# Performance work log

Measured on AMD Instinct MI355X. Metric: run time of the kernel, lower is better.

## Reference

```python
import jax, jax.numpy as jnp
import numpy as np

WS = 8        # window size (square)
TW = 8        # total windows per side = input_resolution // WS
NH = 16       # num heads


def make_indices(ws, tw):
    # local relative position index (N, N)
    c = np.stack(np.meshgrid(np.arange(ws), np.arange(ws), indexing='ij')).reshape(2, -1)
    rel = (c[:, :, None] - c[:, None, :]).transpose(1, 2, 0).astype(np.int64)
    rel[..., 0] += ws - 1
    rel[..., 1] += ws - 1
    rel[..., 0] *= 2 * ws - 1
    local_idx = rel.sum(-1)
    # global (window-token -> window-grid) relative position index (N, tw*tw)
    ck = np.stack(np.meshgrid(np.arange(tw), np.arange(tw), indexing='ij')).reshape(2, -1)
    relg = (c[:, :, None] - ck[:, None, :]).transpose(1, 2, 0).astype(np.int64)
    relg[..., 0] += tw - 1
    relg[..., 1] += tw - 1
    relg[..., 0] *= ws + tw - 1
    global_idx = relg.sum(-1)
    return local_idx, global_idx


def setup_inputs() -> dict:
    key = jax.random.key(0)
    ks = jax.random.split(key, 13)
    B, H, W, C = 16, 64, 64, 512
    s = 0.02
    return {
        'x': jax.random.normal(ks[0], (B, H, W, C), jnp.float32),
        'qkv_w': jax.random.normal(ks[1], (C, 3 * C), jnp.float32) * s,
        'qkv_b': jax.random.normal(ks[2], (3 * C,), jnp.float32) * s,
        'local_bias_table': jax.random.normal(ks[3], ((2 * WS - 1) ** 2, NH), jnp.float32) * s,
        'global_bias_table': jax.random.normal(ks[4], ((WS + TW - 1) ** 2, NH), jnp.float32) * s,
        'local_proj_w': jax.random.normal(ks[5], (C, C), jnp.float32) * s,
        'local_proj_b': jax.random.normal(ks[6], (C,), jnp.float32) * s,
        'pool_w': jnp.full((WS * WS,), 1.0 / (WS * WS) * (WS * WS), jnp.float32) * 0 + jax.random.normal(ks[7], (WS * WS,), jnp.float32) * s + 1.0 / (WS * WS),
        'pool_b': jnp.zeros((1,), jnp.float32),
        'global_proj_w': jax.random.normal(ks[8], (C, C), jnp.float32) * s,
        'global_proj_b': jax.random.normal(ks[9], (C,), jnp.float32) * s,
        'pfc_w': jax.random.normal(ks[10], (2 * C, C), jnp.float32) * s,
        'pfc_b': jax.random.normal(ks[11], (C,), jnp.float32) * s,
    }


def reference(x, qkv_w, qkv_b, local_bias_table, global_bias_table,
              local_proj_w, local_proj_b, pool_w, pool_b,
              global_proj_w, global_proj_b, pfc_w, pfc_b):
    B, H, W, C = x.shape
    N = WS * WS                      # tokens per window
    nWs = (H // WS) * (W // WS)      # number of windows
    B_ = B * nWs
    hd = C // NH
    scale = hd ** -0.5

    local_idx, global_idx = make_indices(WS, H // WS)

    # NOTE: faithful to original — qkv applied to x in row-major order,
    # then reshaped into (B_, N, ...) chunks (window_partition output is unused).
    qkv = (x.reshape(-1, C) @ qkv_w + qkv_b).reshape(B_, N, 3, NH, hd)
    qkv = qkv.transpose(2, 0, 3, 1, 4)  # (3, B_, NH, N, hd)
    q, k, v = qkv[0], qkv[1], qkv[2]

    # ---- fine (local window) attention ----
    lb = local_bias_table[local_idx.reshape(-1)].reshape(N, N, NH).transpose(2, 0, 1)
    fine = jax.nn.softmax(jnp.einsum('bhnd,bhmd->bhnm', q * scale, k) + lb[None])
    fine_out = jnp.einsum('bhnm,bhmd->bnhd', fine, v).reshape(B_, N, C)
    fine_out = fine_out @ local_proj_w + local_proj_b

    # ---- coarse (pooled global) attention ----
    k5 = k.reshape(B, nWs, NH, N, hd)
    v5 = v.reshape(B, nWs, NH, N, hd)
    # pooled over the N window-token axis; original uses pool_layer_k for BOTH K and V
    Kg = jnp.einsum('bwhnd,n->bhwd', k5, pool_w) + pool_b  # (B, NH, nWs, hd)
    Vg = jnp.einsum('bwhnd,n->bhwd', v5, pool_w) + pool_b
    Kb = jnp.broadcast_to(Kg[:, None], (B, nWs, NH, nWs, hd)).reshape(B_, NH, nWs, hd)
    Vb = jnp.broadcast_to(Vg[:, None], (B, nWs, NH, nWs, hd)).reshape(B_, NH, nWs, hd)

    gb = global_bias_table[global_idx.reshape(-1)].reshape(N, nWs, NH).transpose(2, 0, 1)
    coarse = jax.nn.softmax(jnp.einsum('bhnd,bhwd->bhnw', q * scale, Kb) + gb[None])
    coarse_out = jnp.einsum('bhnw,bhwd->bnhd', coarse, Vb).reshape(B_, N, C)
    coarse_out = coarse_out @ global_proj_w + global_proj_b

    # ---- fused projection ----
    out = jnp.concatenate([fine_out, coarse_out], axis=-1) @ pfc_w + pfc_b
    return out  # (B_, N, C)
```

## Files before the change

kernel.cpp:

```cpp
#include <hip/hip_runtime.h>


typedef unsigned int u32;
typedef _Float16 f16;
typedef __attribute__((ext_vector_type(8))) _Float16 f16x8;
typedef __attribute__((ext_vector_type(4))) float f32x4;
typedef __attribute__((ext_vector_type(4))) u32 u32x4;

__device__ __forceinline__ f32x4 mfma_16x16x32(f16x8 a, f16x8 b, f32x4 c) {
  return __builtin_amdgcn_mfma_f32_16x16x32_f16(a, b, c, 0, 0, 0);
}

__device__ __forceinline__ void async_cp16(const void* g, void* l) {
  __builtin_amdgcn_global_load_lds(
      (const __attribute__((address_space(1))) u32*)g,
      (__attribute__((address_space(3))) u32*)l, 16, 0, 0);
}

__device__ __forceinline__ f16x8 cvt8_rtz(const float4 a, const float4 b) {
  u32x4 w;
  w[0] = __builtin_bit_cast(u32, __builtin_amdgcn_cvt_pkrtz(a.x, a.y));
  w[1] = __builtin_bit_cast(u32, __builtin_amdgcn_cvt_pkrtz(a.z, a.w));
  w[2] = __builtin_bit_cast(u32, __builtin_amdgcn_cvt_pkrtz(b.x, b.y));
  w[3] = __builtin_bit_cast(u32, __builtin_amdgcn_cvt_pkrtz(b.z, b.w));
  return __builtin_bit_cast(f16x8, w);
}


__global__ void k_cvtx(const float* __restrict__ X, f16* __restrict__ X16) {
  const size_t stride = (size_t)2048 * 256 * 8;
  size_t base = ((size_t)blockIdx.x * 256 + threadIdx.x) * 8;
  for (int it = 0; it < 8; ++it, base += stride) {
    const float4 a = *reinterpret_cast<const float4*>(X + base);
    const float4 b = *reinterpret_cast<const float4*>(X + base + 4);
    *reinterpret_cast<f16x8*>(X16 + base) = cvt8_rtz(a, b);
  }
}

__global__ void k_biastab(const float* __restrict__ ltab, const float* __restrict__ gtab,
                          float* __restrict__ lbf, float* __restrict__ gbf) {
  const int id = blockIdx.x * 256 + threadIdx.x;
  const int tab = id >> 14;
  const int rem = id & 16383;
  const int h = rem >> 10;
  const int wv = (rem >> 8) & 3;
  const int j = (rem >> 6) & 3;
  const int l = rem & 63;
  const int lk = l >> 4, lr = l & 15;
  const float* src = tab ? gtab : ltab;
  float* out = (tab ? gbf : lbf) + (size_t)rem * 4;
#pragma unroll
  for (int r = 0; r < 4; ++r) {
    const int n = wv * 16 + lk * 4 + r;
    const int m = j * 16 + lr;
    const int idx = ((n >> 3) - (m >> 3) + 7) * 15 + ((n & 7) - (m & 7) + 7);
    out[r] = src[idx * 16 + h];
  }
}

__global__ void k_tqkvw(const float* __restrict__ w, f16* __restrict__ wT) {
  __shared__ f16 sT[64][72];
  const int bid = blockIdx.x;
  const int k0 = (bid / 24) * 64, n0 = (bid % 24) * 64;
  const float sc = (n0 < 512) ? 0.17677669529663687f : 1.0f;
  const int t = threadIdx.x;
#pragma unroll
  for (int p = 0; p < 4; ++p) {
    const int kl = p * 16 + (t >> 4), nl = (t & 15) * 4;
    const float4 v = *reinterpret_cast<const float4*>(w + (size_t)(k0 + kl) * 1536 + n0 + nl);
    sT[kl][nl] = (f16)(v.x * sc); sT[kl][nl + 1] = (f16)(v.y * sc);
    sT[kl][nl + 2] = (f16)(v.z * sc); sT[kl][nl + 3] = (f16)(v.w * sc);
  }
  __syncthreads();
#pragma unroll
  for (int q = 0; q < 2; ++q) {
    const int nl = q * 32 + (t >> 3), kl = (t & 7) * 8;
    f16x8 r;
#pragma unroll
    for (int j = 0; j < 8; ++j) r[j] = sT[kl + j][nl];
    *reinterpret_cast<f16x8*>(wT + (size_t)(n0 + nl) * 512 + k0 + kl) = r;
  }
}

__global__ __launch_bounds__(256) void k_compose(const float* __restrict__ lpw,
                                                 const float* __restrict__ gpw,
                                                 const float* __restrict__ pfc_w,
                                                 f16* __restrict__ WT) {
  __shared__ float sW[16][16];
  const int kk0 = blockIdx.x * 16;
  const bool top = kk0 < 512;
  const float* src = top ? (lpw + kk0 * 512) : (gpw + (kk0 - 512) * 512);
  const float* pf = pfc_w + (top ? 0 : 512 * 512);
  const int t = threadIdx.x;
  float acc0[16], acc1[16];
#pragma unroll
  for (int i = 0; i < 16; ++i) { acc0[i] = 0.f; acc1[i] = 0.f; }
  for (int ct = 0; ct < 32; ++ct) {
    sW[t >> 4][t & 15] = src[(t >> 4) * 512 + ct * 16 + (t & 15)];
    __syncthreads();
#pragma unroll
    for (int cc = 0; cc < 16; ++cc) {
      const int c = ct * 16 + cc;
      const float p0 = pf[c * 512 + t];
      const float p1 = pf[c * 512 + t + 256];
#pragma unroll
      for (int i = 0; i < 16; ++i) { acc0[i] += sW[i][cc] * p0; acc1[i] += sW[i][cc] * p1; }
    }
    __syncthreads();
  }
#pragma unroll
  for (int i = 0; i < 16; ++i) {
    const int kk = kk0 + i;
    const int kp = ((kk >> 5) & 15) * 64 + (kk >> 9) * 32 + (kk & 31);
    WT[(size_t)t * 1024 + kp] = (f16)acc0[i];
    WT[(size_t)(t + 256) * 1024 + kp] = (f16)acc1[i];
  }
}

__global__ void k_bc_init(const float* __restrict__ pfc_b, float* __restrict__ bc) {
  const int j = blockIdx.x * 256 + threadIdx.x;
  bc[j] = pfc_b[j];
}

__global__ void k_bc_acc(const float* __restrict__ lpb, const float* __restrict__ gpb,
                         const float* __restrict__ pfc_w, float* __restrict__ bc) {
  const int t = threadIdx.x;
  const int c0 = blockIdx.x * 32;
  float p0 = 0.f, p1 = 0.f;
#pragma unroll
  for (int i = 0; i < 32; ++i) {
    const int c = c0 + i;
    const float wgt = (c < 512) ? lpb[c] : gpb[c - 512];
    p0 += wgt * pfc_w[(size_t)c * 512 + t];
    p1 += wgt * pfc_w[(size_t)c * 512 + t + 256];
  }
  atomicAdd(bc + t, p0);
  atomicAdd(bc + t + 256, p1);
}

__global__ __launch_bounds__(512, 2) void k_gemm_qkv(const f16* __restrict__ A,
                                                     const f16* __restrict__ BT,
                                                     const float* __restrict__ qkv_b,
                                                     const float* __restrict__ pool_w,
                                                     const float* __restrict__ pool_b,
                                                     f16* __restrict__ qb,
                                                     f16* __restrict__ kb,
                                                     f16* __restrict__ vb,
                                                     f16* __restrict__ Kgb,
                                                     f16* __restrict__ Vgt) {
  __shared__ f16 sA[8192], sB[4096];
  const int wid = (blockIdx.x & 7) * 384 + (blockIdx.x >> 3);
  const int br = wid / 12, bn = wid % 12;
  const int t = threadIdx.x;
  const int wv = t >> 6, l = t & 63, lr = l & 15, lk = l >> 4;
  const int wvr = wv >> 1, wvc = wv & 1;

  f32x4 acc[4][4] = {};

  const f16* gA = A + (size_t)(br * 256 + (t >> 2)) * 512 + (t & 3) * 8;
  const f16* gB = BT + (size_t)(bn * 128 + (t >> 2)) * 512 + (t & 3) * 8;

  for (int kk = 0; kk < 16; ++kk) {
    async_cp16(gA + kk * 32, &sA[t * 8]);
    async_cp16(gA + 128 * 512 + kk * 32, &sA[4096 + t * 8]);
    async_cp16(gB + kk * 32, &sB[t * 8]);
    __syncthreads();
    f16x8 af[4], bf[4];
#pragma unroll
    for (int m = 0; m < 4; ++m)
      af[m] = *reinterpret_cast<const f16x8*>(&sA[(wvr * 64 + m * 16 + lr) * 32 + lk * 8]);
#pragma unroll
    for (int n = 0; n < 4; ++n)
      bf[n] = *reinterpret_cast<const f16x8*>(&sB[(wvc * 64 + n * 16 + lr) * 32 + lk * 8]);
#pragma unroll
    for (int m = 0; m < 4; ++m)
#pragma unroll
      for (int n = 0; n < 4; ++n) acc[m][n] = mfma_16x16x32(af[m], bf[n], acc[m][n]);
    __syncthreads();
  }

  const int w_idx = br * 4 + wvr;
  const int bb = w_idx >> 6, ww = w_idx & 63;
  float pw[4][4];
#pragma unroll
  for (int m = 0; m < 4; ++m)
#pragma unroll
    for (int r = 0; r < 4; ++r) pw[m][r] = pool_w[m * 16 + lk * 4 + r];
  const float pb = pool_b[0];

#pragma unroll
  for (int n = 0; n < 4; ++n) {
    const int col = bn * 128 + wvc * 64 + n * 16 + lr;
    const int which = col >> 9;
    const int hh = (col >> 5) & 15, d = col & 31;
    const float bias = which == 0 ? qkv_b[col] * 0.17677669529663687f : qkv_b[col];
    f16* dst = which == 0 ? qb : (which == 1 ? kb : vb);
#pragma unroll
    for (int m = 0; m < 4; ++m)
#pragma unroll
      for (int r = 0; r < 4; ++r) {
        const int row = br * 256 + wvr * 64 + m * 16 + lk * 4 + r;
        dst[(size_t)(((row >> 6) << 4) + hh) * 2048 + (row & 63) * 32 + d] =
            (f16)(acc[m][n][r] + bias);
      }
    if (which != 0) {
      float part = 0.f;
#pragma unroll
      for (int m = 0; m < 4; ++m)
#pragma unroll
        for (int r = 0; r < 4; ++r) part += (acc[m][n][r] + bias) * pw[m][r];
      part += __shfl_xor(part, 16);
      part += __shfl_xor(part, 32);
      part += pb;
      if (lk == 0) {
        if (which == 1)
          Kgb[((size_t)(bb * 16 + hh) * 64 + ww) * 32 + d] = (f16)part;
        else
          Vgt[((size_t)(bb * 16 + hh) * 32 + d) * 64 + ww] = (f16)part;
      }
    }
  }
}

__global__ __launch_bounds__(256) void k_attn(const f16* __restrict__ qb,
                                              const f16* __restrict__ kb,
                                              const f16* __restrict__ vb,
                                              const f16* __restrict__ Kgb,
                                              const f16* __restrict__ Vgt,
                                              const float* __restrict__ lbf,
                                              const float* __restrict__ gbf,
                                              f16* __restrict__ cat) {
  __shared__ f16 sVraw[2048];
  __shared__ f16 sVt[2048];
  __shared__ f16 sP[4096];
  __shared__ f16 sCat[4096];
  const int bid = blockIdx.x;
  const int b_ = bid >> 4, h = bid & 15;
  const int gs = ((b_ >> 6) << 4) + h;
  const int t = threadIdx.x;
  const int wv = t >> 6, l = t & 63, lr = l & 15, lk = l >> 4;
  const size_t hs = (size_t)bid * 2048;

  async_cp16(vb + hs + t * 8, &sVraw[t * 8]);

  const f16x8 aq = *reinterpret_cast<const f16x8*>(qb + hs + (wv * 16 + lr) * 32 + lk * 8);
  const float* btL = lbf + (size_t)((h * 4 + wv) * 4) * 256 + l * 4;
  const float* btG = gbf + (size_t)((h * 4 + wv) * 4) * 256 + l * 4;

  f32x4 s[4];
#pragma unroll
  for (int j = 0; j < 4; ++j) {
    const f16x8 bk = *reinterpret_cast<const f16x8*>(kb + hs + (j * 16 + lr) * 32 + lk * 8);
    s[j] = mfma_16x16x32(aq, bk, *reinterpret_cast<const f32x4*>(btL + j * 256));
  }

  __syncthreads();

  {
    const int d = t >> 3, tok0 = (t & 7) << 3;
    f16x8 w;
#pragma unroll
    for (int j = 0; j < 8; ++j) w[j] = sVraw[(tok0 + j) * 32 + d];
    *reinterpret_cast<f16x8*>(&sVt[d * 64 + (((t & 7) ^ (d & 7)) << 3)]) = w;
  }

  float p[4][4], inv[4];
#pragma unroll
  for (int r = 0; r < 4; ++r) {
    float su = 0.f;
#pragma unroll
    for (int j = 0; j < 4; ++j) {
      const float e = __expf(s[j][r]);
      p[j][r] = e;
      su += e;
    }
    su += __shfl_xor(su, 1);
    su += __shfl_xor(su, 2);
    su += __shfl_xor(su, 4);
    su += __shfl_xor(su, 8);
    inv[r] = 1.f / su;
  }
#pragma unroll
  for (int r = 0; r < 4; ++r) {
    const int rowP = wv * 16 + lk * 4 + r;
#pragma unroll
    for (int j = 0; j < 4; ++j) {
      const int col = j * 16 + lr;
      sP[rowP * 64 + (((col >> 3) ^ (rowP & 7)) << 3) + (col & 7)] = (f16)p[j][r];
    }
  }

  __syncthreads();

  {
    const int rowP = wv * 16 + lr;
    const f16x8 a0 = *reinterpret_cast<const f16x8*>(&sP[rowP * 64 + ((lk ^ (lr & 7)) << 3)]);
    const f16x8 a1 = *reinterpret_cast<const f16x8*>(&sP[rowP * 64 + (((4 + lk) ^ (lr & 7)) << 3)]);
#pragma unroll
    for (int n = 0; n < 2; ++n) {
      const int d = n * 16 + lr;
      const f16x8 b0 = *reinterpret_cast<const f16x8*>(&sVt[d * 64 + ((lk ^ (d & 7)) << 3)]);
      const f16x8 b1 = *reinterpret_cast<const f16x8*>(&sVt[d * 64 + (((4 + lk) ^ (d & 7)) << 3)]);
      f32x4 o = {};
      o = mfma_16x16x32(a0, b0, o);
      o = mfma_16x16x32(a1, b1, o);
#pragma unroll
      for (int r = 0; r < 4; ++r) {
        const int rowC = wv * 16 + lk * 4 + r;
        const int colC = n * 16 + lr;
        sCat[rowC * 64 + (((colC >> 3) ^ (rowC & 7)) << 3) + (colC & 7)] =
            (f16)(o[r] * inv[r]);
      }
    }
  }

#pragma unroll
  for (int j = 0; j < 4; ++j) {
    const f16x8 bk = *reinterpret_cast<const f16x8*>(
        Kgb + ((size_t)gs * 64 + j * 16 + lr) * 32 + lk * 8);
    s[j] = mfma_16x16x32(aq, bk, *reinterpret_cast<const f32x4*>(btG + j * 256));
  }
#pragma unroll
  for (int r = 0; r < 4; ++r) {
    float su = 0.f;
#pragma unroll
    for (int j = 0; j < 4; ++j) {
      const float e = __expf(s[j][r]);
      p[j][r] = e;
      su += e;
    }
    su += __shfl_xor(su, 1);
    su += __shfl_xor(su, 2);
    su += __shfl_xor(su, 4);
    su += __shfl_xor(su, 8);
    inv[r] = 1.f / su;
  }
#pragma unroll
  for (int r = 0; r < 4; ++r) {
    const int rowP = wv * 16 + lk * 4 + r;
#pragma unroll
    for (int j = 0; j < 4; ++j) {
      const int col = j * 16 + lr;
      sP[rowP * 64 + (((col >> 3) ^ (rowP & 7)) << 3) + (col & 7)] = (f16)p[j][r];
    }
  }

  {
    const int rowP = wv * 16 + lr;
    const f16x8 a0 = *reinterpret_cast<const f16x8*>(&sP[rowP * 64 + ((lk ^ (lr & 7)) << 3)]);
    const f16x8 a1 = *reinterpret_cast<const f16x8*>(&sP[rowP * 64 + (((4 + lk) ^ (lr & 7)) << 3)]);
#pragma unroll
    for (int n = 0; n < 2; ++n) {
      const f16* vp = Vgt + ((size_t)gs * 32 + n * 16 + lr) * 64 + lk * 8;
      const f16x8 b0 = *reinterpret_cast<const f16x8*>(vp);
      const f16x8 b1 = *reinterpret_cast<const f16x8*>(vp + 32);
      f32x4 o = {};
      o = mfma_16x16x32(a0, b0, o);
      o = mfma_16x16x32(a1, b1, o);
#pragma unroll
      for (int r = 0; r < 4; ++r) {
        const int rowC = wv * 16 + lk * 4 + r;
        const int colC = 32 + n * 16 + lr;
        sCat[rowC * 64 + (((colC >> 3) ^ (rowC & 7)) << 3) + (colC & 7)] =
            (f16)(o[r] * inv[r]);
      }
    }
  }

  f16* catp = cat + ((size_t)b_ * 64) * 1024 + h * 64;
#pragma unroll
  for (int pass = 0; pass < 2; ++pass) {
    const int row = wv * 16 + pass * 8 + (l >> 3);
    const int c = l & 7;
    const f16x8 v = *reinterpret_cast<const f16x8*>(&sCat[row * 64 + ((c ^ (row & 7)) << 3)]);
    *reinterpret_cast<f16x8*>(catp + (size_t)row * 1024 + c * 8) = v;
  }
}

__global__ __launch_bounds__(512, 2) void k_gemm_final(const f16* __restrict__ A,
                                                       const f16* __restrict__ BT,
                                                       const float* __restrict__ bc,
                                                       float* __restrict__ out) {
  __shared__ f16 sA[8192];
  __shared__ f16 sB[16384];
  const int wid = (blockIdx.x & 7) * 128 + (blockIdx.x >> 3);
  const int br = wid >> 1, bn = wid & 1;
  const int t = threadIdx.x;
  const int wv = t >> 6, l = t & 63, lr = l & 15, lk = l >> 4;
  const int wvM = wv >> 2, wvN = wv & 3;

  f32x4 acc[4][4] = {};

  const int srow = t >> 3;
  const int scg = (t & 7) ^ (srow & 7);
  const f16* gA = A + (size_t)(br * 128 + srow) * 1024 + scg * 8;
  const f16* gB = BT + (size_t)(bn * 256 + srow) * 1024 + scg * 8;

  for (int kk = 0; kk < 16; ++kk) {
#pragma unroll
    for (int i = 0; i < 2; ++i)
      async_cp16(gA + (size_t)(i * 64) * 1024 + kk * 64, &sA[(i * 512 + t) * 8]);
#pragma unroll
    for (int i = 0; i < 4; ++i)
      async_cp16(gB + (size_t)(i * 64) * 1024 + kk * 64, &sB[(i * 512 + t) * 8]);
    __syncthreads();
    f16x8 af[4][2], bf[4][2];
#pragma unroll
    for (int m = 0; m < 4; ++m) {
      const int row = wvM * 64 + m * 16 + lr;
#pragma unroll
      for (int hh = 0; hh < 2; ++hh)
        af[m][hh] = *reinterpret_cast<const f16x8*>(
            &sA[row * 64 + ((((hh << 2) + lk) ^ (row & 7)) << 3)]);
    }
#pragma unroll
    for (int n = 0; n < 4; ++n) {
      const int row = wvN * 64 + n * 16 + lr;
#pragma unroll
      for (int hh = 0; hh < 2; ++hh)
        bf[n][hh] = *reinterpret_cast<const f16x8*>(
            &sB[row * 64 + ((((hh << 2) + lk) ^ (row & 7)) << 3)]);
    }
#pragma unroll
    for (int m = 0; m < 4; ++m)
#pragma unroll
      for (int n = 0; n < 4; ++n) {
        acc[m][n] = mfma_16x16x32(af[m][0], bf[n][0], acc[m][n]);
        acc[m][n] = mfma_16x16x32(af[m][1], bf[n][1], acc[m][n]);
      }
    __syncthreads();
  }

#pragma unroll
  for (int n = 0; n < 4; ++n) {
    const int col = bn * 256 + wvN * 64 + n * 16 + lr;
    const float bias = bc[col];
#pragma unroll
    for (int m = 0; m < 4; ++m)
#pragma unroll
      for (int r = 0; r < 4; ++r) {
        const int row = br * 128 + wvM * 64 + m * 16 + lk * 4 + r;
        out[(size_t)row * 512 + col] = acc[m][n][r] + bias;
      }
  }
}


extern "C" void kernel_launch(void* const* d_in, const int* in_sizes, int n_in,
                              void* d_out, int out_size, void* d_ws, size_t ws_size,
                              hipStream_t stream) {
  const float* x      = (const float*)d_in[0];
  const float* qkv_w  = (const float*)d_in[1];
  const float* qkv_b  = (const float*)d_in[2];
  const float* ltab   = (const float*)d_in[3];
  const float* gtab   = (const float*)d_in[4];
  const float* lpw    = (const float*)d_in[5];
  const float* lpb    = (const float*)d_in[6];
  const float* pool_w = (const float*)d_in[7];
  const float* pool_b = (const float*)d_in[8];
  const float* gpw    = (const float*)d_in[9];
  const float* gpb    = (const float*)d_in[10];
  const float* pfc_w  = (const float*)d_in[11];
  const float* pfc_b  = (const float*)d_in[12];
  float* out = (float*)d_out;

  char* ws = (char*)d_ws;
  f16*   qb   = (f16*)(ws + 0);
  f16*   kb   = (f16*)(ws + 67108864);
  f16*   vb   = (f16*)(ws + 134217728);
  f16*   cat  = (f16*)(ws + 201326592);
  f16*   X16  = (f16*)(ws + 201326592);
  f16*   qwT  = (f16*)(ws + 335544320);
  f16*   WcT  = (f16*)(ws + 337117184);
  float* bc   = (float*)(ws + 338165760);
  float* lbf  = (float*)(ws + 338167808);
  float* gbf  = (float*)(ws + 338429952);
  f16*   Kgb  = (f16*)(ws + 338692096);
  f16*   Vgt  = (f16*)(ws + 339740672);

  k_cvtx<<<2048, 256, 0, stream>>>(x, X16);
  k_biastab<<<128, 256, 0, stream>>>(ltab, gtab, lbf, gbf);
  k_tqkvw<<<192, 256, 0, stream>>>(qkv_w, qwT);
  k_compose<<<64, 256, 0, stream>>>(lpw, gpw, pfc_w, WcT);
  k_bc_init<<<2, 256, 0, stream>>>(pfc_b, bc);
  k_bc_acc<<<32, 256, 0, stream>>>(lpb, gpb, pfc_w, bc);
  k_gemm_qkv<<<3072, 512, 0, stream>>>(X16, qwT, qkv_b, pool_w, pool_b,
                                       qb, kb, vb, Kgb, Vgt);
  k_attn<<<16384, 256, 0, stream>>>(qb, kb, vb, Kgb, Vgt, lbf, gbf, cat);
  k_gemm_final<<<1024, 512, 0, stream>>>(cat, WcT, bc, out);
}
```

Measured before the change: 484.9 us.

## Merge prep kernels, double-buffer QKV GEMM, process two windows per attention block

New measurement: 449.6 us. -7.3%, faster.

```diff
diff --git a/kernel.cpp b/kernel.cpp
--- a/kernel.cpp
+++ b/kernel.cpp
@@ -26,116 +26,103 @@
   return __builtin_bit_cast(f16x8, w);
 }
 
-
-__global__ void k_cvtx(const float* __restrict__ X, f16* __restrict__ X16) {
-  const size_t stride = (size_t)2048 * 256 * 8;
-  size_t base = ((size_t)blockIdx.x * 256 + threadIdx.x) * 8;
-  for (int it = 0; it < 8; ++it, base += stride) {
-    const float4 a = *reinterpret_cast<const float4*>(X + base);
-    const float4 b = *reinterpret_cast<const float4*>(X + base + 4);
-    *reinterpret_cast<f16x8*>(X16 + base) = cvt8_rtz(a, b);
-  }
-}
-
-__global__ void k_biastab(const float* __restrict__ ltab, const float* __restrict__ gtab,
-                          float* __restrict__ lbf, float* __restrict__ gbf) {
-  const int id = blockIdx.x * 256 + threadIdx.x;
-  const int tab = id >> 14;
-  const int rem = id & 16383;
-  const int h = rem >> 10;
-  const int wv = (rem >> 8) & 3;
-  const int j = (rem >> 6) & 3;
-  const int l = rem & 63;
-  const int lk = l >> 4, lr = l & 15;
-  const float* src = tab ? gtab : ltab;
-  float* out = (tab ? gbf : lbf) + (size_t)rem * 4;
-#pragma unroll
-  for (int r = 0; r < 4; ++r) {
-    const int n = wv * 16 + lk * 4 + r;
-    const int m = j * 16 + lr;
-    const int idx = ((n >> 3) - (m >> 3) + 7) * 15 + ((n & 7) - (m & 7) + 7);
-    out[r] = src[idx * 16 + h];
-  }
-}
-
-__global__ void k_tqkvw(const float* __restrict__ w, f16* __restrict__ wT) {
-  __shared__ f16 sT[64][72];
-  const int bid = blockIdx.x;
-  const int k0 = (bid / 24) * 64, n0 = (bid % 24) * 64;
-  const float sc = (n0 < 512) ? 0.17677669529663687f : 1.0f;
+__global__ __launch_bounds__(256) void k_prep(
+    const float* __restrict__ X, f16* __restrict__ X16,
+    const float* __restrict__ ltab, const float* __restrict__ gtab,
+    float* __restrict__ lbf, float* __restrict__ gbf,
+    const float* __restrict__ qkv_w, f16* __restrict__ qwT,
+    const float* __restrict__ lpw, const float* __restrict__ gpw,
+    const float* __restrict__ pfc_w, f16* __restrict__ WcT,
+    const float* __restrict__ lpb, const float* __restrict__ gpb,
+    const float* __restrict__ pfc_b, float* __restrict__ bc) {
+  __shared__ char sm[9216];
+  const int b = blockIdx.x;
   const int t = threadIdx.x;
-#pragma unroll
-  for (int p = 0; p < 4; ++p) {
-    const int kl = p * 16 + (t >> 4), nl = (t & 15) * 4;
-    const float4 v = *reinterpret_cast<const float4*>(w + (size_t)(k0 + kl) * 1536 + n0 + nl);
-    sT[kl][nl] = (f16)(v.x * sc); sT[kl][nl + 1] = (f16)(v.y * sc);
-    sT[kl][nl + 2] = (f16)(v.z * sc); sT[kl][nl + 3] = (f16)(v.w * sc);
-  }
-  __syncthreads();
-#pragma unroll
-  for (int q = 0; q < 2; ++q) {
-    const int nl = q * 32 + (t >> 3), kl = (t & 7) * 8;
-    f16x8 r;
-#pragma unroll
-    for (int j = 0; j < 8; ++j) r[j] = sT[kl + j][nl];
-    *reinterpret_cast<f16x8*>(wT + (size_t)(n0 + nl) * 512 + k0 + kl) = r;
-  }
-}
-
-__global__ __launch_bounds__(256) void k_compose(const float* __restrict__ lpw,
-                                                 const float* __restrict__ gpw,
-                                                 const float* __restrict__ pfc_w,
-                                                 f16* __restrict__ WT) {
-  __shared__ float sW[16][16];
-  const int kk0 = blockIdx.x * 16;
-  const bool top = kk0 < 512;
-  const float* src = top ? (lpw + kk0 * 512) : (gpw + (kk0 - 512) * 512);
-  const float* pf = pfc_w + (top ? 0 : 512 * 512);
-  const int t = threadIdx.x;
-  float acc0[16], acc1[16];
-#pragma unroll
-  for (int i = 0; i < 16; ++i) { acc0[i] = 0.f; acc1[i] = 0.f; }
-  for (int ct = 0; ct < 32; ++ct) {
-    sW[t >> 4][t & 15] = src[(t >> 4) * 512 + ct * 16 + (t & 15)];
+
+  if (b < 64) {
+    float (*sW)[16] = (float(*)[16])sm;
+    const int kk0 = b * 16;
+    const bool top = kk0 < 512;
+    const float* src = top ? (lpw + kk0 * 512) : (gpw + (kk0 - 512) * 512);
+    const float* pf = pfc_w + (top ? 0 : 512 * 512);
+    float acc0[16], acc1[16];
+#pragma unroll
+    for (int i = 0; i < 16; ++i) { acc0[i] = 0.f; acc1[i] = 0.f; }
+    for (int ct = 0; ct < 32; ++ct) {
+      sW[t >> 4][t & 15] = src[(t >> 4) * 512 + ct * 16 + (t & 15)];
+      __syncthreads();
+#pragma unroll
+      for (int cc = 0; cc < 16; ++cc) {
+        const int c = ct * 16 + cc;
+        const float p0 = pf[c * 512 + t];
+        const float p1 = pf[c * 512 + t + 256];
+#pragma unroll
+        for (int i = 0; i < 16; ++i) { acc0[i] += sW[i][cc] * p0; acc1[i] += sW[i][cc] * p1; }
+      }
+      __syncthreads();
+    }
+#pragma unroll
+    for (int i = 0; i < 16; ++i) {
+      const int kk = kk0 + i;
+      const int kp = ((kk >> 5) & 15) * 64 + (kk >> 9) * 32 + (kk & 31);
+      WcT[(size_t)t * 1024 + kp] = (f16)acc0[i];
+      WcT[(size_t)(t + 256) * 1024 + kp] = (f16)acc1[i];
+    }
+  } else if (b < 66) {
+    const int j = (b - 64) * 256 + t;
+    float acc = pfc_b[j];
+    for (int c = 0; c < 512; ++c)
+      acc += lpb[c] * pfc_w[(size_t)c * 512 + j] + gpb[c] * pfc_w[(size_t)(512 + c) * 512 + j];
+    bc[j] = acc;
+  } else if (b < 194) {
+    const int id = (b - 66) * 256 + t;
+    const int tab = id >> 14;
+    const int rem = id & 16383;
+    const int h = rem >> 10;
+    const int wv = (rem >> 8) & 3;
+    const int j = (rem >> 6) & 3;
+    const int l = rem & 63;
+    const int lk = l >> 4, lr = l & 15;
+    const float* src = tab ? gtab : ltab;
+    float* out = (tab ? gbf : lbf) + (size_t)rem * 4;
+#pragma unroll
+    for (int r = 0; r < 4; ++r) {
+      const int n = wv * 16 + lk * 4 + r;
+      const int m = j * 16 + lr;
+      const int idx = ((n >> 3) - (m >> 3) + 7) * 15 + ((n & 7) - (m & 7) + 7);
+      out[r] = src[idx * 16 + h];
+    }
+  } else if (b < 386) {
+    f16 (*sT)[72] = (f16(*)[72])sm;
+    const int bid = b - 194;
+    const int k0 = (bid / 24) * 64, n0 = (bid % 24) * 64;
+    const float sc = (n0 < 512) ? 0.17677669529663687f : 1.0f;
+#pragma unroll
+    for (int p = 0; p < 4; ++p) {
+      const int kl = p * 16 + (t >> 4), nl = (t & 15) * 4;
+      const float4 v = *reinterpret_cast<const float4*>(qkv_w + (size_t)(k0 + kl) * 1536 + n0 + nl);
+      sT[kl][nl] = (f16)(v.x * sc); sT[kl][nl + 1] = (f16)(v.y * sc);
+      sT[kl][nl + 2] = (f16)(v.z * sc); sT[kl][nl + 3] = (f16)(v.w * sc);
+    }
     __syncthreads();
 #pragma unroll
-    for (int cc = 0; cc < 16; ++cc) {
-      const int c = ct * 16 + cc;
-      const float p0 = pf[c * 512 + t];
-      const float p1 = pf[c * 512 + t + 256];
-#pragma unroll
-      for (int i = 0; i < 16; ++i) { acc0[i] += sW[i][cc] * p0; acc1[i] += sW[i][cc] * p1; }
-    }
-    __syncthreads();
-  }
-#pragma unroll
-  for (int i = 0; i < 16; ++i) {
-    const int kk = kk0 + i;
-    const int kp = ((kk >> 5) & 15) * 64 + (kk >> 9) * 32 + (kk & 31);
-    WT[(size_t)t * 1024 + kp] = (f16)acc0[i];
-    WT[(size_t)(t + 256) * 1024 + kp] = (f16)acc1[i];
-  }
-}
-
-__global__ void k_bc_init(const float* __restrict__ pfc_b, float* __restrict__ bc) {
-  const int j = blockIdx.x * 256 + threadIdx.x;
-  bc[j] = pfc_b[j];
-}
-
-__global__ void k_bc_acc(const float* __restrict__ lpb, const float* __restrict__ gpb,
-                         const float* __restrict__ pfc_w, float* __restrict__ bc) {
-  const int t = threadIdx.x;
-  const int c0 = blockIdx.x * 32;
-  float p0 = 0.f, p1 = 0.f;
-#pragma unroll
-  for (int i = 0; i < 32; ++i) {
-    const int c = c0 + i;
-    const float wgt = (c < 512) ? lpb[c] : gpb[c - 512];
-    p0 += wgt * pfc_w[(size_t)c * 512 + t];
-    p1 += wgt * pfc_w[(size_t)c * 512 + t + 256];
-  }
-  atomicAdd(bc + t, p0);
-  atomicAdd(bc + t + 256, p1);
+    for (int q = 0; q < 2; ++q) {
+      const int nl = q * 32 + (t >> 3), kl = (t & 7) * 8;
+      f16x8 r;
+#pragma unroll
+      for (int j = 0; j < 8; ++j) r[j] = sT[kl + j][nl];
+      *reinterpret_cast<f16x8*>(qwT + (size_t)(n0 + nl) * 512 + k0 + kl) = r;
+    }
+  } else {
+    const int vb = b - 386;
+    const size_t stride = (size_t)2048 * 256 * 8;
+    size_t base = ((size_t)vb * 256 + t) * 8;
+    for (int it = 0; it < 8; ++it, base += stride) {
+      const float4 a = *reinterpret_cast<const float4*>(X + base);
+      const float4 bb = *reinterpret_cast<const float4*>(X + base + 4);
+      *reinterpret_cast<f16x8*>(X16 + base) = cvt8_rtz(a, bb);
+    }
+  }
 }
 
 __global__ __launch_bounds__(512, 2) void k_gemm_qkv(const f16* __restrict__ A,
@@ -148,7 +135,7 @@
                                                      f16* __restrict__ vb,
                                                      f16* __restrict__ Kgb,
                                                      f16* __restrict__ Vgt) {
-  __shared__ f16 sA[8192], sB[4096];
+  __shared__ f16 sA[2][8192], sB[2][4096];
   const int wid = (blockIdx.x & 7) * 384 + (blockIdx.x >> 3);
   const int br = wid / 12, bn = wid % 12;
   const int t = threadIdx.x;
@@ -160,23 +147,33 @@
   const f16* gA = A + (size_t)(br * 256 + (t >> 2)) * 512 + (t & 3) * 8;
   const f16* gB = BT + (size_t)(bn * 128 + (t >> 2)) * 512 + (t & 3) * 8;
 
+  async_cp16(gA, &sA[0][t * 8]);
+  async_cp16(gA + 128 * 512, &sA[0][4096 + t * 8]);
+  async_cp16(gB, &sB[0][t * 8]);
+  __syncthreads();
+
+  int cur = 0;
   for (int kk = 0; kk < 16; ++kk) {
-    async_cp16(gA + kk * 32, &sA[t * 8]);
-    async_cp16(gA + 128 * 512 + kk * 32, &sA[4096 + t * 8]);
-    async_cp16(gB + kk * 32, &sB[t * 8]);
-    __syncthreads();
+    if (kk < 15) {
+      async_cp16(gA + (kk + 1) * 32, &sA[cur ^ 1][t * 8]);
+      async_cp16(gA + 128 * 512 + (kk + 1) * 32, &sA[cur ^ 1][4096 + t * 8]);
+      async_cp16(gB + (kk + 1) * 32, &sB[cur ^ 1][t * 8]);
+    }
     f16x8 af[4], bf[4];
 #pragma unroll
     for (int m = 0; m < 4; ++m)
-      af[m] = *reinterpret_cast<const f16x8*>(&sA[(wvr * 64 + m * 16 + lr) * 32 + lk * 8]);
+      af[m] = *reinterpret_cast<const f16x8*>(&sA[cur][(wvr * 64 + m * 16 + lr) * 32 + lk * 8]);
 #pragma unroll
     for (int n = 0; n < 4; ++n)
-      bf[n] = *reinterpret_cast<const f16x8*>(&sB[(wvc * 64 + n * 16 + lr) * 32 + lk * 8]);
+      bf[n] = *reinterpret_cast<const f16x8*>(&sB[cur][(wvc * 64 + n * 16 + lr) * 32 + lk * 8]);
 #pragma unroll
     for (int m = 0; m < 4; ++m)
 #pragma unroll
       for (int n = 0; n < 4; ++n) acc[m][n] = mfma_16x16x32(af[m], bf[n], acc[m][n]);
-    __syncthreads();
+    if (kk < 15) {
+      __syncthreads();
+      cur ^= 1;
+    }
   }
 
   const int w_idx = br * 4 + wvr;
@@ -230,150 +227,167 @@
                                               const float* __restrict__ lbf,
                                               const float* __restrict__ gbf,
                                               f16* __restrict__ cat) {
-  __shared__ f16 sVraw[2048];
-  __shared__ f16 sVt[2048];
-  __shared__ f16 sP[4096];
-  __shared__ f16 sCat[4096];
+  __shared__ f16 sVrawA[2048], sVrawB[2048];
+  __shared__ f16 sVtA[2048], sVtB[2048];
+  __shared__ f16 sP[4096], sCat[4096];
   const int bid = blockIdx.x;
-  const int b_ = bid >> 4, h = bid & 15;
-  const int gs = ((b_ >> 6) << 4) + h;
+  const int h = bid >> 9, pair = bid & 511;
+  const int b_0 = pair * 2;
+  const int gs = ((b_0 >> 6) << 4) + h;
   const int t = threadIdx.x;
   const int wv = t >> 6, l = t & 63, lr = l & 15, lk = l >> 4;
-  const size_t hs = (size_t)bid * 2048;
-
-  async_cp16(vb + hs + t * 8, &sVraw[t * 8]);
-
-  const f16x8 aq = *reinterpret_cast<const f16x8*>(qb + hs + (wv * 16 + lr) * 32 + lk * 8);
-  const float* btL = lbf + (size_t)((h * 4 + wv) * 4) * 256 + l * 4;
-  const float* btG = gbf + (size_t)((h * 4 + wv) * 4) * 256 + l * 4;
-
-  f32x4 s[4];
+  const size_t hs0 = ((size_t)b_0 * 16 + h) * 2048;
+  const size_t hs1 = hs0 + 16 * 2048;
+
+  async_cp16(vb + hs0 + t * 8, &sVrawA[t * 8]);
+  async_cp16(vb + hs1 + t * 8, &sVrawB[t * 8]);
+
+  f32x4 bL[4], bG[4];
 #pragma unroll
   for (int j = 0; j < 4; ++j) {
-    const f16x8 bk = *reinterpret_cast<const f16x8*>(kb + hs + (j * 16 + lr) * 32 + lk * 8);
-    s[j] = mfma_16x16x32(aq, bk, *reinterpret_cast<const f32x4*>(btL + j * 256));
-  }
-
-  __syncthreads();
-
-  {
-    const int d = t >> 3, tok0 = (t & 7) << 3;
-    f16x8 w;
-#pragma unroll
-    for (int j = 0; j < 8; ++j) w[j] = sVraw[(tok0 + j) * 32 + d];
-    *reinterpret_cast<f16x8*>(&sVt[d * 64 + (((t & 7) ^ (d & 7)) << 3)]) = w;
+    bL[j] = *reinterpret_cast<const f32x4*>(lbf + (size_t)((h * 4 + wv) * 4 + j) * 256 + l * 4);
+    bG[j] = *reinterpret_cast<const f32x4*>(gbf + (size_t)((h * 4 + wv) * 4 + j) * 256 + l * 4);
   }
 
   float p[4][4], inv[4];
-#pragma unroll
-  for (int r = 0; r < 4; ++r) {
-    float su = 0.f;
+
+#pragma unroll
+  for (int w = 0; w < 2; ++w) {
+    const size_t hs = w ? hs1 : hs0;
+    const f16* sVt = w ? sVtB : sVtA;
+    const f16x8 aq = *reinterpret_cast<const f16x8*>(qb + hs + (wv * 16 + lr) * 32 + lk * 8);
+
+    f32x4 s[4];
 #pragma unroll
     for (int j = 0; j < 4; ++j) {
-      const float e = __expf(s[j][r]);
-      p[j][r] = e;
-      su += e;
-    }
-    su += __shfl_xor(su, 1);
-    su += __shfl_xor(su, 2);
-    su += __shfl_xor(su, 4);
-    su += __shfl_xor(su, 8);
-    inv[r] = 1.f / su;
-  }
-#pragma unroll
-  for (int r = 0; r < 4; ++r) {
-    const int rowP = wv * 16 + lk * 4 + r;
+      const f16x8 bk = *reinterpret_cast<const f16x8*>(kb + hs + (j * 16 + lr) * 32 + lk * 8);
+      s[j] = mfma_16x16x32(aq, bk, bL[j]);
+    }
+
+    if (w == 0) {
+      __syncthreads();
+      const int d = t >> 3, tok0 = (t & 7) << 3;
+      f16x8 wa, wb;
+#pragma unroll
+      for (int j = 0; j < 8; ++j) {
+        wa[j] = sVrawA[(tok0 + j) * 32 + d];
+        wb[j] = sVrawB[(tok0 + j) * 32 + d];
+      }
+      const int slot = d * 64 + (((t & 7) ^ (d & 7)) << 3);
+      *reinterpret_cast<f16x8*>(&sVtA[slot]) = wa;
+      *reinterpret_cast<f16x8*>(&sVtB[slot]) = wb;
+    }
+
+#pragma unroll
+    for (int r = 0; r < 4; ++r) {
+      float su = 0.f;
+#pragma unroll
+      for (int j = 0; j < 4; ++j) {
+        const float e = __expf(s[j][r]);
+        p[j][r] = e;
+        su += e;
+      }
+      su += __shfl_xor(su, 1);
+      su += __shfl_xor(su, 2);
+      su += __shfl_xor(su, 4);
+      su += __shfl_xor(su, 8);
+      inv[r] = 1.f / su;
+    }
+#pragma unroll
+    for (int r = 0; r < 4; ++r) {
+      const int rowP = wv * 16 + lk * 4 + r;
+#pragma unroll
+      for (int j = 0; j < 4; ++j) {
+        const int col = j * 16 + lr;
+        sP[rowP * 64 + (((col >> 3) ^ (rowP & 7)) << 3) + (col & 7)] = (f16)p[j][r];
+      }
+    }
+
+    if (w == 0) __syncthreads();
+
+    {
+      const int rowP = wv * 16 + lr;
+      const f16x8 a0 = *reinterpret_cast<const f16x8*>(&sP[rowP * 64 + ((lk ^ (lr & 7)) << 3)]);
+      const f16x8 a1 = *reinterpret_cast<const f16x8*>(&sP[rowP * 64 + (((4 + lk) ^ (lr & 7)) << 3)]);
+#pragma unroll
+      for (int n = 0; n < 2; ++n) {
+        const int d = n * 16 + lr;
+        const f16x8 b0 = *reinterpret_cast<const f16x8*>(&sVt[d * 64 + ((lk ^ (d & 7)) << 3)]);
+        const f16x8 b1 = *reinterpret_cast<const f16x8*>(&sVt[d * 64 + (((4 + lk) ^ (d & 7)) << 3)]);
+        f32x4 o = {};
+        o = mfma_16x16x32(a0, b0, o);
+        o = mfma_16x16x32(a1, b1, o);
+#pragma unroll
+        for (int r = 0; r < 4; ++r) {
+          const int rowC = wv * 16 + lk * 4 + r;
+          const int colC = n * 16 + lr;
+          sCat[rowC * 64 + (((colC >> 3) ^ (rowC & 7)) << 3) + (colC & 7)] =
+              (f16)(o[r] * inv[r]);
+        }
+      }
+    }
+
 #pragma unroll
     for (int j = 0; j < 4; ++j) {
-      const int col = j * 16 + lr;
-      sP[rowP * 64 + (((col >> 3) ^ (rowP & 7)) << 3) + (col & 7)] = (f16)p[j][r];
-    }
-  }
-
-  __syncthreads();
-
-  {
-    const int rowP = wv * 16 + lr;
-    const f16x8 a0 = *reinterpret_cast<const f16x8*>(&sP[rowP * 64 + ((lk ^ (lr & 7)) << 3)]);
-    const f16x8 a1 = *reinterpret_cast<const f16x8*>(&sP[rowP * 64 + (((4 + lk) ^ (lr & 7)) << 3)]);
-#pragma unroll
-    for (int n = 0; n < 2; ++n) {
-      const int d = n * 16 + lr;
-      const f16x8 b0 = *reinterpret_cast<const f16x8*>(&sVt[d * 64 + ((lk ^ (d & 7)) << 3)]);
-      const f16x8 b1 = *reinterpret_cast<const f16x8*>(&sVt[d * 64 + (((4 + lk) ^ (d & 7)) << 3)]);
-      f32x4 o = {};
-      o = mfma_16x16x32(a0, b0, o);
-      o = mfma_16x16x32(a1, b1, o);
-#pragma unroll
-      for (int r = 0; r < 4; ++r) {
-        const int rowC = wv * 16 + lk * 4 + r;
-        const int colC = n * 16 + lr;
-        sCat[rowC * 64 + (((colC >> 3) ^ (rowC & 7)) << 3) + (colC & 7)] =
-            (f16)(o[r] * inv[r]);
-      }
-    }
-  }
-
-#pragma unroll
-  for (int j = 0; j < 4; ++j) {
-    const f16x8 bk = *reinterpret_cast<const f16x8*>(
-        Kgb + ((size_t)gs * 64 + j * 16 + lr) * 32 + lk * 8);
-    s[j] = mfma_16x16x32(aq, bk, *reinterpret_cast<const f32x4*>(btG + j * 256));
-  }
-#pragma unroll
-  for (int r = 0; r < 4; ++r) {
-    float su = 0.f;
-#pragma unroll
-    for (int j = 0; j < 4; ++j) {
-      const float e = __expf(s[j][r]);
-      p[j][r] = e;
-      su += e;
-    }
-    su += __shfl_xor(su, 1);
-    su += __shfl_xor(su, 2);
-    su += __shfl_xor(su, 4);
-    su += __shfl_xor(su, 8);
-    inv[r] = 1.f / su;
-  }
-#pragma unroll
-  for (int r = 0; r < 4; ++r) {
-    const int rowP = wv * 16 + lk * 4 + r;
-#pragma unroll
-    for (int j = 0; j < 4; ++j) {
-      const int col = j * 16 + lr;
-      sP[rowP * 64 + (((col >> 3) ^ (rowP & 7)) << 3) + (col & 7)] = (f16)p[j][r];
-    }
-  }
-
-  {
-    const int rowP = wv * 16 + lr;
-    const f16x8 a0 = *reinterpret_cast<const f16x8*>(&sP[rowP * 64 + ((lk ^ (lr & 7)) << 3)]);
-    const f16x8 a1 = *reinterpret_cast<const f16x8*>(&sP[rowP * 64 + (((4 + lk) ^ (lr & 7)) << 3)]);
-#pragma unroll
-    for (int n = 0; n < 2; ++n) {
-      const f16* vp = Vgt + ((size_t)gs * 32 + n * 16 + lr) * 64 + lk * 8;
-      const f16x8 b0 = *reinterpret_cast<const f16x8*>(vp);
-      const f16x8 b1 = *reinterpret_cast<const f16x8*>(vp + 32);
-      f32x4 o = {};
-      o = mfma_16x16x32(a0, b0, o);
-      o = mfma_16x16x32(a1, b1, o);
-#pragma unroll
-      for (int r = 0; r < 4; ++r) {
-        const int rowC = wv * 16 + lk * 4 + r;
-        const int colC = 32 + n * 16 + lr;
-        sCat[rowC * 64 + (((colC >> 3) ^ (rowC & 7)) << 3) + (colC & 7)] =
-            (f16)(o[r] * inv[r]);
-      }
-    }
-  }
-
-  f16* catp = cat + ((size_t)b_ * 64) * 1024 + h * 64;
-#pragma unroll
-  for (int pass = 0; pass < 2; ++pass) {
-    const int row = wv * 16 + pass * 8 + (l >> 3);
-    const int c = l & 7;
-    const f16x8 v = *reinterpret_cast<const f16x8*>(&sCat[row * 64 + ((c ^ (row & 7)) << 3)]);
-    *reinterpret_cast<f16x8*>(catp + (size_t)row * 1024 + c * 8) = v;
+      const f16x8 bk = *reinterpret_cast<const f16x8*>(
+          Kgb + ((size_t)gs * 64 + j * 16 + lr) * 32 + lk * 8);
+      s[j] = mfma_16x16x32(aq, bk, bG[j]);
+    }
+#pragma unroll
+    for (int r = 0; r < 4; ++r) {
+      float su = 0.f;
+#pragma unroll
+      for (int j = 0; j < 4; ++j) {
+        const float e = __expf(s[j][r]);
+        p[j][r] = e;
+        su += e;
+      }
+      su += __shfl_xor(su, 1);
+      su += __shfl_xor(su, 2);
+      su += __shfl_xor(su, 4);
+      su += __shfl_xor(su, 8);
+      inv[r] = 1.f / su;
+    }
+#pragma unroll
+    for (int r = 0; r < 4; ++r) {
+      const int rowP = wv * 16 + lk * 4 + r;
+#pragma unroll
+      for (int j = 0; j < 4; ++j) {
+        const int col = j * 16 + lr;
+        sP[rowP * 64 + (((col >> 3) ^ (rowP & 7)) << 3) + (col & 7)] = (f16)p[j][r];
+      }
+    }
+
+    {
+      const int rowP = wv * 16 + lr;
+      const f16x8 a0 = *reinterpret_cast<const f16x8*>(&sP[rowP * 64 + ((lk ^ (lr & 7)) << 3)]);
+      const f16x8 a1 = *reinterpret_cast<const f16x8*>(&sP[rowP * 64 + (((4 + lk) ^ (lr & 7)) << 3)]);
+#pragma unroll
+      for (int n = 0; n < 2; ++n) {
+        const f16* vp = Vgt + ((size_t)gs * 32 + n * 16 + lr) * 64 + lk * 8;
+        const f16x8 b0 = *reinterpret_cast<const f16x8*>(vp);
+        const f16x8 b1 = *reinterpret_cast<const f16x8*>(vp + 32);
+        f32x4 o = {};
+        o = mfma_16x16x32(a0, b0, o);
+        o = mfma_16x16x32(a1, b1, o);
+#pragma unroll
+        for (int r = 0; r < 4; ++r) {
+          const int rowC = wv * 16 + lk * 4 + r;
+          const int colC = 32 + n * 16 + lr;
+          sCat[rowC * 64 + (((colC >> 3) ^ (rowC & 7)) << 3) + (colC & 7)] =
+              (f16)(o[r] * inv[r]);
+        }
+      }
+    }
+
+    f16* catp = cat + ((size_t)(b_0 + w) * 64) * 1024 + h * 64;
+#pragma unroll
+    for (int pass = 0; pass < 2; ++pass) {
+      const int row = wv * 16 + pass * 8 + (l >> 3);
+      const int c = l & 7;
+      const f16x8 v = *reinterpret_cast<const f16x8*>(&sCat[row * 64 + ((c ^ (row & 7)) << 3)]);
+      *reinterpret_cast<f16x8*>(catp + (size_t)row * 1024 + c * 8) = v;
+    }
   }
 }
 
@@ -478,14 +492,10 @@
   f16*   Kgb  = (f16*)(ws + 338692096);
   f16*   Vgt  = (f16*)(ws + 339740672);
 
-  k_cvtx<<<2048, 256, 0, stream>>>(x, X16);
-  k_biastab<<<128, 256, 0, stream>>>(ltab, gtab, lbf, gbf);
-  k_tqkvw<<<192, 256, 0, stream>>>(qkv_w, qwT);
-  k_compose<<<64, 256, 0, stream>>>(lpw, gpw, pfc_w, WcT);
-  k_bc_init<<<2, 256, 0, stream>>>(pfc_b, bc);
-  k_bc_acc<<<32, 256, 0, stream>>>(lpb, gpb, pfc_w, bc);
+  k_prep<<<2434, 256, 0, stream>>>(x, X16, ltab, gtab, lbf, gbf, qkv_w, qwT,
+                                   lpw, gpw, pfc_w, WcT, lpb, gpb, pfc_b, bc);
   k_gemm_qkv<<<3072, 512, 0, stream>>>(X16, qwT, qkv_b, pool_w, pool_b,
                                        qb, kb, vb, Kgb, Vgt);
-  k_attn<<<16384, 256, 0, stream>>>(qb, kb, vb, Kgb, Vgt, lbf, gbf, cat);
+  k_attn<<<8192, 256, 0, stream>>>(qb, kb, vb, Kgb, Vgt, lbf, gbf, cat);
   k_gemm_final<<<1024, 512, 0, stream>>>(cat, WcT, bc, out);
 }
```
